# Performance work log

Hardware: AMD Instinct MI355X
Metric: run time of the kernel (lower is better)

## Reference

```python
import jax, jax.numpy as jnp
import numpy as np
import math

# (mul, l, parity) triples for irreps_in1 == irreps_in2 == '32x0e+16x1o+8x2e'
IRREPS = [(32, 0, 1), (16, 1, -1), (8, 2, 1)]
BATCH = 2048


def _fact(n):
    return math.factorial(n)


def _w3j_entry(j1, j2, j3, m1, m2, m3):
    # Racah formula for the (complex-basis) Wigner 3j symbol, integer l's.
    if m1 + m2 + m3 != 0:
        return 0.0
    t_min = max(0, j2 - j3 - m1, j1 - j3 + m2)
    t_max = min(j1 + j2 - j3, j1 - m1, j2 + m2)
    if t_max < t_min:
        return 0.0
    s = 0.0
    for t in range(t_min, t_max + 1):
        s += (-1) ** t / (
            _fact(t) * _fact(j3 - j2 + t + m1) * _fact(j3 - j1 + t - m2)
            * _fact(j1 + j2 - j3 - t) * _fact(j1 - t - m1) * _fact(j2 - t + m2))
    delta = math.sqrt(_fact(j1 + j2 - j3) * _fact(j1 - j2 + j3)
                      * _fact(-j1 + j2 + j3) / _fact(j1 + j2 + j3 + 1))
    pref = math.sqrt(_fact(j1 + m1) * _fact(j1 - m1) * _fact(j2 + m2)
                     * _fact(j2 - m2) * _fact(j3 + m3) * _fact(j3 - m3))
    return (-1) ** (j1 - j2 - m3) * delta * pref * s


def _w3j_complex(j1, j2, j3):
    W = np.zeros((2 * j1 + 1, 2 * j2 + 1, 2 * j3 + 1))
    for m1 in range(-j1, j1 + 1):
        for m2 in range(-j2, j2 + 1):
            m3 = -(m1 + m2)
            if abs(m3) <= j3:
                W[m1 + j1, m2 + j2, m3 + j3] = _w3j_entry(j1, j2, j3, m1, m2, m3)
    return W


def _c2r(l):
    # complex -> real spherical harmonic change-of-basis (rows: real m, cols: complex mu)
    U = np.zeros((2 * l + 1, 2 * l + 1), dtype=np.complex128)
    U[l, l] = 1.0
    rs2 = 1.0 / math.sqrt(2.0)
    for m in range(1, l + 1):
        U[l + m, l + m] = (-1) ** m * rs2
        U[l + m, l - m] = rs2
        U[l - m, l - m] = 1j * rs2
        U[l - m, l + m] = -1j * (-1) ** m * rs2
    return U


def _w3j_real(l1, l2, l3):
    # Wigner 3j in the real spherical-harmonic basis (same sparsity/math as e3nn o3.wigner_3j)
    W = _w3j_complex(l1, l2, l3).astype(np.complex128)
    C = np.einsum('abc,ia,jb,kc->ijk', W, _c2r(l1), _c2r(l2), _c2r(l3))
    if np.linalg.norm(C.imag) > np.linalg.norm(C.real):
        C = np.ascontiguousarray(C.imag)
    else:
        C = np.ascontiguousarray(C.real)
    C[np.abs(C) < 1e-12] = 0.0
    return C


def _build_structure():
    # Mirrors CudaTensorProduct.__init__ with irreps_out=None: enumerate every
    # then emit sparse COO entries (in1_idx, in2_idx, out_idx, cb_val).
    entries_by_l3 = {}
    off1 = 0
    for mul1, l1, p1 in IRREPS:
        off2_base = 0
        for mul2, l2, p2 in IRREPS:
            for l3 in range(abs(l1 - l2), l1 + l2 + 1):
                p3 = (p1 * p2 + 1) // 2
                o1 = off1
                for _i in range(mul1):
                    o2 = off2_base
                    for _j in range(mul2):
                        entries_by_l3.setdefault((l3, p3), []).append((l1, l2, o1, o2))
                        o2 += 2 * l2 + 1
                    o1 += 2 * l1 + 1
            off2_base += (2 * l2 + 1) * mul2
        off1 += (2 * l1 + 1) * mul1

    l3s = sorted(entries_by_l3.keys(), key=lambda x: 2 * (x[0] + 1) + x[1])
    in1_idx, in2_idx, out_idx, cb_vals = [], [], [], []
    row = 0
    w3j_cache = {}
    for l3, p3 in l3s:
        for l1, l2, o1, o2 in entries_by_l3[(l3, p3)]:
            key = (l1, l2, l3)
            if key not in w3j_cache:
                w3j_cache[key] = _w3j_real(l1, l2, l3)
            C = w3j_cache[key]
            scale = math.sqrt(2 * l3 + 1)
            for m3 in range(2 * l3 + 1):
                for m2 in range(2 * l2 + 1):
                    for m1 in range(2 * l1 + 1):
                        v = C[m1, m2, m3]
                        if v == 0.0:
                            continue
                        in1_idx.append(m1 + o1)
                        in2_idx.append(m2 + o2)
                        out_idx.append(m3 + row)
                        cb_vals.append(float(v * scale))
            row += 2 * l3 + 1

    # palette/index encoding, as in the module (palette[0] == 0 is the filler slot)
    palette = sorted(set(cb_vals))
    palette.insert(0, 0.0)
    lut = {v: i for i, v in enumerate(palette)}
    cb_idx = [lut[v] for v in cb_vals]
    return (np.asarray(in1_idx, np.int32), np.asarray(in2_idx, np.int32),
            np.asarray(out_idx, np.int32), np.asarray(cb_idx, np.int32),
            np.asarray(palette, np.float32), row)


def setup_inputs() -> dict:
    key = jax.random.key(0)
    k1, k2 = jax.random.split(key)
    i1, i2, io, ic, pal, cb_height = _build_structure()
    dim = sum(m * (2 * l + 1) for m, l, _ in IRREPS)  # 120
    return {
        'in1': jax.random.normal(k1, (BATCH, dim), jnp.float32),
        'in2': jax.random.normal(k2, (BATCH, dim), jnp.float32),
        'cb_palette': jnp.asarray(pal),
        'in1_indices': jnp.asarray(i1),
        'in2_indices': jnp.asarray(i2),
        'out_indices': jnp.asarray(io),
        'cb_indices': jnp.asarray(ic),
        'cb_height': int(cb_height),
    }


def reference(in1, in2, cb_palette, in1_indices, in2_indices, out_indices, cb_indices, cb_height):
    # intermediate[b, o] = sum_k palette[cb_idx[k]] * in1[b, i1[k]] * in2[b, i2[k]]
    vals = cb_palette[cb_indices]                                   # [K]
    contrib = in1[:, in1_indices] * in2[:, in2_indices] * vals[None, :]  # [B, K]
    # scatter-accumulate along the sparse output rows
    out = jax.ops.segment_sum(contrib.T, out_indices, num_segments=cb_height).T  # [B, cb_height]
    return out
```

## Files before the change

kernel.cpp:

```cpp
#include <hip/hip_runtime.h>

#define DIM 120
#define NB 16
#define NBP 20
#define BLOCK 256
#define NG (NB / 4)

__global__ void pre_kernel(const int* __restrict__ out_idx, int K, int H,
                           int* __restrict__ row_start,
                           const int* __restrict__ i1, const int* __restrict__ i2,
                           const int* __restrict__ cb, const float* __restrict__ pal,
                           uint2* __restrict__ ent) {
    int t = blockIdx.x * blockDim.x + threadIdx.x;
    if (t <= H) {
        int lo = 0, hi = K;
        while (lo < hi) {
            int mid = (lo + hi) >> 1;
            if (out_idx[mid] < t) lo = mid + 1; else hi = mid;
        }
        row_start[t] = lo;
    }
    if (t < K) {
        uint2 e;
        e.x = (unsigned)i1[t] | ((unsigned)i2[t] << 16);
        e.y = __float_as_uint(pal[cb[t]]);
        ent[t] = e;
    }
}

__global__ __launch_bounds__(BLOCK, 8) void tp_kernel(
    const float* __restrict__ in1, const float* __restrict__ in2,
    const uint2* __restrict__ ent, const int* __restrict__ row_start,
    float* __restrict__ out, int H) {
    __shared__ __align__(16) float s1t[DIM * NBP];
    __shared__ __align__(16) float s2t[DIM * NBP];

    const int b0 = blockIdx.y * NB;
    for (int t = threadIdx.x; t < 2 * DIM * NG; t += BLOCK) {
        const int arr = (t >= DIM * NG);
        const int c = arr ? t - DIM * NG : t;
        const int d = c % DIM;
        const int g = c / DIM;
        const float* __restrict__ src = arr ? in2 : in1;
        const size_t base = (size_t)(b0 + 4 * g) * DIM + d;
        float4 v;
        v.x = src[base + 0 * DIM];
        v.y = src[base + 1 * DIM];
        v.z = src[base + 2 * DIM];
        v.w = src[base + 3 * DIM];
        float* dst = arr ? s2t : s1t;
        *(float4*)(dst + d * NBP + 4 * g) = v;
    }
    __syncthreads();

    const int o = blockIdx.x * BLOCK + threadIdx.x;
    if (o >= H) return;
    const int k0 = row_start[o];
    const int k1 = row_start[o + 1];

    float acc[NB];
#pragma unroll
    for (int b = 0; b < NB; ++b) acc[b] = 0.0f;

    for (int k = k0; k < k1; ++k) {
        const uint2 e = ent[k];
        const float4* __restrict__ pa = (const float4*)(s1t + (e.x & 0xffffu) * NBP);
        const float4* __restrict__ pc = (const float4*)(s2t + (e.x >> 16) * NBP);
        const float v = __uint_as_float(e.y);
#pragma unroll
        for (int j = 0; j < NG; ++j) {
            const float4 x = pa[j];
            const float4 y = pc[j];
            acc[4 * j + 0] = fmaf(v * x.x, y.x, acc[4 * j + 0]);
            acc[4 * j + 1] = fmaf(v * x.y, y.y, acc[4 * j + 1]);
            acc[4 * j + 2] = fmaf(v * x.z, y.z, acc[4 * j + 2]);
            acc[4 * j + 3] = fmaf(v * x.w, y.w, acc[4 * j + 3]);
        }
    }

#pragma unroll
    for (int b = 0; b < NB; ++b)
        out[(size_t)(b0 + b) * H + o] = acc[b];
}

extern "C" void kernel_launch(void* const* d_in, const int* in_sizes, int n_in,
                              void* d_out, int out_size, void* d_ws, size_t ws_size,
                              hipStream_t stream) {
    const float* in1 = (const float*)d_in[0];
    const float* in2 = (const float*)d_in[1];
    const float* pal = (const float*)d_in[2];
    const int*   i1  = (const int*)d_in[3];
    const int*   i2  = (const int*)d_in[4];
    const int*   oi  = (const int*)d_in[5];
    const int*   cb  = (const int*)d_in[6];

    const int K = in_sizes[3];
    const int B = in_sizes[0] / DIM;
    const int H = out_size / B;

    uint2* ent = (uint2*)d_ws;
    int* row_start = (int*)((char*)d_ws + (size_t)K * sizeof(uint2));

    {
        const int n = (K > H + 1) ? K : (H + 1);
        pre_kernel<<<(n + 255) / 256, 256, 0, stream>>>(oi, K, H, row_start,
                                                        i1, i2, cb, pal, ent);
    }

    dim3 grid((H + BLOCK - 1) / BLOCK, B / NB);
    tp_kernel<<<grid, BLOCK, 0, stream>>>(in1, in2, ent, row_start,
                                          (float*)d_out, H);
}
```

Before: 34.44 us.

## Assign four output rows per thread with swizzled 8-batch shared tiles

Each thread now computes four consecutive output rows for 8 batch elements instead of one row for 16. This allows vectorized float4 stores and loads of row_start. Shared-memory tiles switch to a 32-byte-per-dim layout with an XOR swizzle, and the byte offsets are precomputed into the entry table. The aim is fewer bank conflicts and wider global writes. The trade-off is that the smaller batch tile re-reads the entry table twice as often and loads more input tiles, and the rows handled by one thread are uneven in length. The code assumes H is a multiple of 4 for aligned int4/float4 accesses.

```diff
diff --git a/kernel.cpp b/kernel.cpp
--- a/kernel.cpp
+++ b/kernel.cpp
@@ -1,10 +1,14 @@
 #include <hip/hip_runtime.h>
 
 #define DIM 120
-#define NB 16
-#define NBP 20
+#define NB 8
+#define RQ 4
 #define BLOCK 256
-#define NG (NB / 4)
+#define ROWS_PER_BLOCK (BLOCK * RQ)
+
+__device__ __host__ __forceinline__ int swzoff(int idx) {
+    return (idx ^ ((idx >> 2) & 3)) << 5;
+}
 
 __global__ void pre_kernel(const int* __restrict__ out_idx, int K, int H,
                            int* __restrict__ row_start,
@@ -22,65 +26,77 @@
     }
     if (t < K) {
         uint2 e;
-        e.x = (unsigned)i1[t] | ((unsigned)i2[t] << 16);
+        e.x = (unsigned)swzoff(i1[t]) | ((unsigned)swzoff(i2[t]) << 16);
         e.y = __float_as_uint(pal[cb[t]]);
         ent[t] = e;
     }
 }
 
-__global__ __launch_bounds__(BLOCK, 8) void tp_kernel(
+__global__ __launch_bounds__(BLOCK) void tp_kernel(
     const float* __restrict__ in1, const float* __restrict__ in2,
     const uint2* __restrict__ ent, const int* __restrict__ row_start,
     float* __restrict__ out, int H) {
-    __shared__ __align__(16) float s1t[DIM * NBP];
-    __shared__ __align__(16) float s2t[DIM * NBP];
+    __shared__ __align__(16) float s1t[DIM * NB];
+    __shared__ __align__(16) float s2t[DIM * NB];
 
     const int b0 = blockIdx.y * NB;
-    for (int t = threadIdx.x; t < 2 * DIM * NG; t += BLOCK) {
-        const int arr = (t >= DIM * NG);
-        const int c = arr ? t - DIM * NG : t;
-        const int d = c % DIM;
-        const int g = c / DIM;
+    for (int t = threadIdx.x; t < 2 * DIM * (NB / 4); t += BLOCK) {
+        const int arr = (t >= DIM * (NB / 4));
+        const int c = arr ? t - DIM * (NB / 4) : t;
+        const int d = c >> 1;
+        const int bg = c & 1;
         const float* __restrict__ src = arr ? in2 : in1;
-        const size_t base = (size_t)(b0 + 4 * g) * DIM + d;
+        const size_t base = (size_t)(b0 + 4 * bg) * DIM + d;
         float4 v;
         v.x = src[base + 0 * DIM];
         v.y = src[base + 1 * DIM];
         v.z = src[base + 2 * DIM];
         v.w = src[base + 3 * DIM];
-        float* dst = arr ? s2t : s1t;
-        *(float4*)(dst + d * NBP + 4 * g) = v;
+        char* dst = (char*)(arr ? s2t : s1t);
+        *(float4*)(dst + swzoff(d) + 16 * bg) = v;
     }
     __syncthreads();
 
-    const int o = blockIdx.x * BLOCK + threadIdx.x;
-    if (o >= H) return;
-    const int k0 = row_start[o];
-    const int k1 = row_start[o + 1];
+    const int o0 = blockIdx.x * ROWS_PER_BLOCK + (int)threadIdx.x * RQ;
+    if (o0 >= H) return;
 
-    float acc[NB];
+    int rs[RQ + 1];
+    *(int4*)rs = *(const int4*)(row_start + o0);
+    rs[RQ] = row_start[o0 + RQ];
+
+    float acc[RQ][NB];
 #pragma unroll
-    for (int b = 0; b < NB; ++b) acc[b] = 0.0f;
+    for (int r = 0; r < RQ; ++r)
+#pragma unroll
+        for (int b = 0; b < NB; ++b) acc[r][b] = 0.0f;
 
-    for (int k = k0; k < k1; ++k) {
-        const uint2 e = ent[k];
-        const float4* __restrict__ pa = (const float4*)(s1t + (e.x & 0xffffu) * NBP);
-        const float4* __restrict__ pc = (const float4*)(s2t + (e.x >> 16) * NBP);
-        const float v = __uint_as_float(e.y);
 #pragma unroll
-        for (int j = 0; j < NG; ++j) {
-            const float4 x = pa[j];
-            const float4 y = pc[j];
-            acc[4 * j + 0] = fmaf(v * x.x, y.x, acc[4 * j + 0]);
-            acc[4 * j + 1] = fmaf(v * x.y, y.y, acc[4 * j + 1]);
-            acc[4 * j + 2] = fmaf(v * x.z, y.z, acc[4 * j + 2]);
-            acc[4 * j + 3] = fmaf(v * x.w, y.w, acc[4 * j + 3]);
+    for (int r = 0; r < RQ; ++r) {
+        for (int k = rs[r]; k < rs[r + 1]; ++k) {
+            const uint2 e = ent[k];
+            const char* p1 = (const char*)s1t + (e.x & 0xffffu);
+            const char* p2 = (const char*)s2t + (e.x >> 16);
+            const float4 x0 = *(const float4*)(p1);
+            const float4 x1 = *(const float4*)(p1 + 16);
+            const float4 y0 = *(const float4*)(p2);
+            const float4 y1 = *(const float4*)(p2 + 16);
+            const float v = __uint_as_float(e.y);
+            acc[r][0] = fmaf(v * x0.x, y0.x, acc[r][0]);
+            acc[r][1] = fmaf(v * x0.y, y0.y, acc[r][1]);
+            acc[r][2] = fmaf(v * x0.z, y0.z, acc[r][2]);
+            acc[r][3] = fmaf(v * x0.w, y0.w, acc[r][3]);
+            acc[r][4] = fmaf(v * x1.x, y1.x, acc[r][4]);
+            acc[r][5] = fmaf(v * x1.y, y1.y, acc[r][5]);
+            acc[r][6] = fmaf(v * x1.z, y1.z, acc[r][6]);
+            acc[r][7] = fmaf(v * x1.w, y1.w, acc[r][7]);
         }
     }
 
 #pragma unroll
-    for (int b = 0; b < NB; ++b)
-        out[(size_t)(b0 + b) * H + o] = acc[b];
+    for (int b = 0; b < NB; ++b) {
+        float4 o4 = make_float4(acc[0][b], acc[1][b], acc[2][b], acc[3][b]);
+        *(float4*)(out + (size_t)(b0 + b) * H + o0) = o4;
+    }
 }
 
 extern "C" void kernel_launch(void* const* d_in, const int* in_sizes, int n_in,
@@ -107,7 +123,7 @@
                                                         i1, i2, cb, pal, ent);
     }
 
-    dim3 grid((H + BLOCK - 1) / BLOCK, B / NB);
+    dim3 grid((H + ROWS_PER_BLOCK - 1) / ROWS_PER_BLOCK, B / NB);
     tp_kernel<<<grid, BLOCK, 0, stream>>>(in1, in2, ent, row_start,
                                           (float*)d_out, H);
 }
```

New measurement: 46.15 us. +34.0%, slower.
